# Kernel tuning notes

Hardware: AMD Instinct MI355X
Metric: run time of the kernel (lower is better)

Reference implementation:

```python
import jax, jax.numpy as jnp
import numpy as np

DISTANCE_WEIGHT = 1.001  # self.distence_weight in the torch module


def setup_inputs() -> dict:
    key = jax.random.key(0)
    k1, k2 = jax.random.split(key)
    B, DIM_IN, DIM_OUT = 1024, 512, 512
    x = jax.random.normal(k1, (B, DIM_IN), dtype=jnp.float32)
    centers = jax.random.normal(k2, (DIM_OUT, DIM_IN), dtype=jnp.float32)
    beta = jnp.ones((DIM_OUT,), dtype=jnp.float32)
    return {"x": x, "centers": centers, "beta": beta}


def reference(x, centers, beta):
    # L1 pairwise distance: [B, dim_out]
    sim = jnp.sum(jnp.abs(x[:, None, :] - centers[None, :, :]), axis=-1)
    # negate, shift by global max * distance_weight, scale by beta
    sim = -sim + jnp.max(sim) * DISTANCE_WEIGHT
    return beta * sim
```

## Files before the change

kernel.cpp:

```cpp
#include <hip/hip_runtime.h>


typedef float f4 __attribute__((ext_vector_type(4)));

#define DIM_K 512
#define DIM_O 512
#define W_DIST 1.001f

__global__ __launch_bounds__(256, 2) void k_sim(const float* __restrict__ X,
                                                const float* __restrict__ C,
                                                float* __restrict__ S,
                                                float* __restrict__ bmax)
{
    __shared__ __align__(16) f4 xs[2][8 * 65 + 1];
    const int tid = threadIdx.x;
    const int lane = tid & 63;
    const int wv = __builtin_amdgcn_readfirstlane(tid >> 6);
    const int row0 = (blockIdx.x >> 5) * 64;
    const int col0 = (blockIdx.x & 31) * 16;
    const int o0 = col0 + wv * 4;
    const float* Crow = C + o0 * DIM_K;

    const int srow = tid >> 3;
    const int skg = tid & 7;
    const float* xg0 = X + (row0 + srow) * DIM_K + skg * 4;
    f4 pre0 = *(const f4*)xg0;
    f4 pre1 = *(const f4*)(xg0 + 32 * DIM_K);

    float acc0 = 0.f, acc1 = 0.f, acc2 = 0.f, acc3 = 0.f;

    for (int t = 0; t < 16; ++t) {
        f4* buf = xs[t & 1];
        buf[skg * 65 + srow] = pre0;
        buf[skg * 65 + srow + 32] = pre1;
        if (t < 15) {
            const float* xg = xg0 + (t + 1) * 32;
            pre0 = *(const f4*)xg;
            pre1 = *(const f4*)(xg + 32 * DIM_K);
        }
        __syncthreads();

        const int kc = t * 32;
#pragma unroll
        for (int h = 0; h < 2; ++h) {
            f4 c0[4], c1[4], c2[4], c3[4];
#pragma unroll
            for (int kg = 0; kg < 4; ++kg) {
                const int ko = kc + h * 16 + kg * 4;
                c0[kg] = *(const f4*)(Crow + 0 * DIM_K + ko);
                c1[kg] = *(const f4*)(Crow + 1 * DIM_K + ko);
                c2[kg] = *(const f4*)(Crow + 2 * DIM_K + ko);
                c3[kg] = *(const f4*)(Crow + 3 * DIM_K + ko);
            }
#pragma unroll
            for (int kg = 0; kg < 4; ++kg) {
                const f4 xv = buf[(h * 4 + kg) * 65 + lane];
#pragma unroll
                for (int e = 0; e < 4; ++e) {
                    const float x = xv[e];
                    acc0 += __builtin_fabsf(x - c0[kg][e]);
                    acc1 += __builtin_fabsf(x - c1[kg][e]);
                    acc2 += __builtin_fabsf(x - c2[kg][e]);
                    acc3 += __builtin_fabsf(x - c3[kg][e]);
                }
            }
        }
        __syncthreads();
    }

    f4 out; out[0] = acc0; out[1] = acc1; out[2] = acc2; out[3] = acc3;
    *(f4*)(S + (row0 + lane) * DIM_O + o0) = out;

    float m = fmaxf(fmaxf(acc0, acc1), fmaxf(acc2, acc3));
#pragma unroll
    for (int off = 32; off > 0; off >>= 1)
        m = fmaxf(m, __shfl_xor(m, off, 64));
    __shared__ float wm[4];
    if (lane == 0) wm[tid >> 6] = m;
    __syncthreads();
    if (tid == 0)
        bmax[blockIdx.x] = fmaxf(fmaxf(wm[0], wm[1]), fmaxf(wm[2], wm[3]));
}

__global__ __launch_bounds__(256) void k_out(float* __restrict__ S,
                                             const float* __restrict__ beta,
                                             const float* __restrict__ bmax)
{
    const int tid = threadIdx.x;
    const int lane = tid & 63;
    float m = 0.f;
#pragma unroll
    for (int i = 0; i < 8; ++i)
        m = fmaxf(m, bmax[lane + 64 * i]);
#pragma unroll
    for (int off = 32; off > 0; off >>= 1)
        m = fmaxf(m, __shfl_xor(m, off, 64));
    const float shift = m * W_DIST;

    const int f = blockIdx.x * 256 + tid;
    f4 s = ((const f4*)S)[f];
    f4 b = ((const f4*)beta)[f & 127];
    f4 r;
    r[0] = b[0] * (shift - s[0]);
    r[1] = b[1] * (shift - s[1]);
    r[2] = b[2] * (shift - s[2]);
    r[3] = b[3] * (shift - s[3]);
    ((f4*)S)[f] = r;
}

extern "C" void kernel_launch(void* const* d_in, const int* in_sizes, int n_in,
                              void* d_out, int out_size, void* d_ws, size_t ws_size,
                              hipStream_t stream) {
    const float* X = (const float*)d_in[0];
    const float* C = (const float*)d_in[1];
    const float* beta = (const float*)d_in[2];
    float* S = (float*)d_out;
    float* bmax = (float*)d_ws;
    k_sim<<<512, 256, 0, stream>>>(X, C, S, bmax);
    k_out<<<512, 256, 0, stream>>>(S, beta, bmax);
}
```

Before: 92.56 us.

## Split K across lanes with register-resident X tile and LDS cross-lane reduction

Restructures the L1-distance kernel so each wave's 64 lanes each own 8 K-elements of 8 batch rows, held in registers, and loop over 8 centers. Per-lane partial sums are reduced through a shared-memory transpose plus shuffles instead of the previous shared-memory staged X tiles with per-thread full-K accumulation. The grid grows to 2048 blocks with higher occupancy, and the max kernel now scans 2048 block maxima. In exchange, each center gets an LDS write/read reduction pass, and the L1 arithmetic per loaded center value is lower, so the loop may become bound by reduction overhead.

Result: faster. 83.43 us (-9.9%).

```diff
diff --git a/kernel.cpp b/kernel.cpp
--- a/kernel.cpp
+++ b/kernel.cpp
@@ -7,79 +7,74 @@
 #define DIM_O 512
 #define W_DIST 1.001f
 
-__global__ __launch_bounds__(256, 2) void k_sim(const float* __restrict__ X,
+__global__ __launch_bounds__(256, 4) void k_sim(const float* __restrict__ X,
                                                 const float* __restrict__ C,
                                                 float* __restrict__ S,
                                                 float* __restrict__ bmax)
 {
-    __shared__ __align__(16) f4 xs[2][8 * 65 + 1];
+    __shared__ float part[4][64 * 12];
+    __shared__ float wmx[4];
     const int tid = threadIdx.x;
     const int lane = tid & 63;
-    const int wv = __builtin_amdgcn_readfirstlane(tid >> 6);
-    const int row0 = (blockIdx.x >> 5) * 64;
-    const int col0 = (blockIdx.x & 31) * 16;
-    const int o0 = col0 + wv * 4;
-    const float* Crow = C + o0 * DIM_K;
+    const int wv = tid >> 6;
+    const int bt = blockIdx.x >> 4;
+    const int ob = blockIdx.x & 15;
+    const int b0 = bt * 8;
+    const int o0 = ob * 32 + wv * 8;
+    const int myb = lane >> 3, myo = lane & 7;
 
-    const int srow = tid >> 3;
-    const int skg = tid & 7;
-    const float* xg0 = X + (row0 + srow) * DIM_K + skg * 4;
-    f4 pre0 = *(const f4*)xg0;
-    f4 pre1 = *(const f4*)(xg0 + 32 * DIM_K);
+    f4 xa[8], xb[8];
+    {
+        const float* xp = X + b0 * DIM_K + lane * 8;
+#pragma unroll
+        for (int i = 0; i < 8; ++i) {
+            xa[i] = *(const f4*)(xp + i * DIM_K);
+            xb[i] = *(const f4*)(xp + i * DIM_K + 4);
+        }
+    }
 
-    float acc0 = 0.f, acc1 = 0.f, acc2 = 0.f, acc3 = 0.f;
+    float* mypart = part[wv];
+    float res = 0.f;
 
-    for (int t = 0; t < 16; ++t) {
-        f4* buf = xs[t & 1];
-        buf[skg * 65 + srow] = pre0;
-        buf[skg * 65 + srow + 32] = pre1;
-        if (t < 15) {
-            const float* xg = xg0 + (t + 1) * 32;
-            pre0 = *(const f4*)xg;
-            pre1 = *(const f4*)(xg + 32 * DIM_K);
-        }
-        __syncthreads();
-
-        const int kc = t * 32;
 #pragma unroll
-        for (int h = 0; h < 2; ++h) {
-            f4 c0[4], c1[4], c2[4], c3[4];
+    for (int oc = 0; oc < 8; ++oc) {
+        const float* cp = C + (o0 + oc) * DIM_K + lane * 8;
+        const f4 ca = *(const f4*)cp;
+        const f4 cb = *(const f4*)(cp + 4);
+        f4 aca = {0.f, 0.f, 0.f, 0.f};
+        f4 acb = {0.f, 0.f, 0.f, 0.f};
 #pragma unroll
-            for (int kg = 0; kg < 4; ++kg) {
-                const int ko = kc + h * 16 + kg * 4;
-                c0[kg] = *(const f4*)(Crow + 0 * DIM_K + ko);
-                c1[kg] = *(const f4*)(Crow + 1 * DIM_K + ko);
-                c2[kg] = *(const f4*)(Crow + 2 * DIM_K + ko);
-                c3[kg] = *(const f4*)(Crow + 3 * DIM_K + ko);
-            }
+        for (int e = 0; e < 4; ++e) {
 #pragma unroll
-            for (int kg = 0; kg < 4; ++kg) {
-                const f4 xv = buf[(h * 4 + kg) * 65 + lane];
-#pragma unroll
-                for (int e = 0; e < 4; ++e) {
-                    const float x = xv[e];
-                    acc0 += __builtin_fabsf(x - c0[kg][e]);
-                    acc1 += __builtin_fabsf(x - c1[kg][e]);
-                    acc2 += __builtin_fabsf(x - c2[kg][e]);
-                    acc3 += __builtin_fabsf(x - c3[kg][e]);
-                }
+            for (int i = 0; i < 4; ++i) {
+                aca[i] += __builtin_fabsf(xa[i][e] - ca[e]);
+                aca[i] += __builtin_fabsf(xb[i][e] - cb[e]);
+                acb[i] += __builtin_fabsf(xa[i + 4][e] - ca[e]);
+                acb[i] += __builtin_fabsf(xb[i + 4][e] - cb[e]);
             }
         }
-        __syncthreads();
+        *(f4*)&mypart[lane * 12]     = aca;
+        *(f4*)&mypart[lane * 12 + 4] = acb;
+        float s = 0.f;
+#pragma unroll
+        for (int j = 0; j < 8; ++j)
+            s += mypart[(myo * 8 + j) * 12 + myb];
+        s += __shfl_xor(s, 1, 64);
+        s += __shfl_xor(s, 2, 64);
+        s += __shfl_xor(s, 4, 64);
+        res = (myo == oc) ? s : res;
     }
 
-    f4 out; out[0] = acc0; out[1] = acc1; out[2] = acc2; out[3] = acc3;
-    *(f4*)(S + (row0 + lane) * DIM_O + o0) = out;
+    S[(b0 + myb) * DIM_O + o0 + myo] = res;
 
-    float m = fmaxf(fmaxf(acc0, acc1), fmaxf(acc2, acc3));
+    float m = res;
 #pragma unroll
     for (int off = 32; off > 0; off >>= 1)
         m = fmaxf(m, __shfl_xor(m, off, 64));
-    __shared__ float wm[4];
-    if (lane == 0) wm[tid >> 6] = m;
+    if (lane == 0) wmx[wv] = m;
     __syncthreads();
     if (tid == 0)
-        bmax[blockIdx.x] = fmaxf(fmaxf(wm[0], wm[1]), fmaxf(wm[2], wm[3]));
+        bmax[blockIdx.x] = fmaxf(fmaxf(wmx[0], wmx[1]), fmaxf(wmx[2], wmx[3]));
 }
 
 __global__ __launch_bounds__(256) void k_out(float* __restrict__ S,
@@ -90,7 +85,7 @@
     const int lane = tid & 63;
     float m = 0.f;
 #pragma unroll
-    for (int i = 0; i < 8; ++i)
+    for (int i = 0; i < 32; ++i)
         m = fmaxf(m, bmax[lane + 64 * i]);
 #pragma unroll
     for (int off = 32; off > 0; off >>= 1)
@@ -116,6 +111,6 @@
     const float* beta = (const float*)d_in[2];
     float* S = (float*)d_out;
     float* bmax = (float*)d_ws;
-    k_sim<<<512, 256, 0, stream>>>(X, C, S, bmax);
+    k_sim<<<2048, 256, 0, stream>>>(X, C, S, bmax);
     k_out<<<512, 256, 0, stream>>>(S, beta, bmax);
 }
```
